# Performance work log

Hardware: AMD Instinct MI355X
Metric: run time of the kernel (lower is better)

Reference implementation:

```python
import jax, jax.numpy as jnp
import numpy as np

B, N, D = 8, 2048, 768
H = 12
HD = D // H
W = 16          # window_size
HOP = 8         # hop_size
GB = N // 2 + 1   # global freq bins = 1025
LB = W // 2 + 1   # local freq bins = 9
NW = (N - W) // HOP + 1  # num windows = 255
EPS_LN = 1e-5


def setup_inputs() -> dict:
    key = jax.random.key(0)
    ks = jax.random.split(key, 12)
    s = 0.02
    return {
        "x": jax.random.normal(ks[0], (B, N, D), dtype=jnp.float32),
        "base_filter_global": jnp.ones((H, GB, 1), jnp.float32),
        "base_filter_local": jnp.ones((H, LB, 1), jnp.float32),
        "modrelu_bias_global": jnp.full((H, GB, 1), -0.1, jnp.float32),
        "modrelu_bias_local": jnp.full((H, LB, 1), -0.1, jnp.float32),
        "w1g": jax.random.normal(ks[1], (D, D), jnp.float32) * s,
        "b1g": jnp.zeros((D,), jnp.float32),
        "w2g": jax.random.normal(ks[2], (D, H * GB), jnp.float32) * s,
        "b2g": jnp.zeros((H * GB,), jnp.float32),
        "w1l": jax.random.normal(ks[3], (D, D), jnp.float32) * s,
        "b1l": jnp.zeros((D,), jnp.float32),
        "w2l": jax.random.normal(ks[4], (D, H * LB), jnp.float32) * s,
        "b2l": jnp.zeros((H * LB,), jnp.float32),
        "fusion_w": jax.random.normal(ks[5], (2,), jnp.float32) * 0.5,
        "ln_gamma": jnp.ones((D,), jnp.float32),
        "ln_beta": jnp.zeros((D,), jnp.float32),
    }


def _modrelu(z, bias):
    # modReLU: ReLU(|z| + b) * z / |z|  (|z| clamped at 1e-6 in denominator)
    a = jnp.abs(z)
    return z * (jax.nn.relu(a + bias) / jnp.maximum(a, 1e-6))


def _hann(w):
    # torch.hann_window default (periodic=True)
    n = jnp.arange(w, dtype=jnp.float32)
    return 0.5 * (1.0 - jnp.cos(2.0 * jnp.pi * n / w))


def reference(x, base_filter_global, base_filter_local, modrelu_bias_global,
              modrelu_bias_local, w1g, b1g, w2g, b2g, w1l, b1l, w2l, b2l,
              fusion_w, ln_gamma, ln_beta):
    b, n, d = x.shape
    x_heads = x.reshape(b, n, H, HD).transpose(0, 2, 1, 3)  # (B,H,N,hd)

    # ---- global branch ----
    Fg = jnp.fft.rfft(x_heads, axis=2, norm='ortho')  # (B,H,GB,hd) complex
    ctx = x.mean(axis=1)  # (B,D)
    mg = jnp.tanh(jax.nn.gelu(ctx @ w1g + b1g, approximate=False) @ w2g + b2g)
    mg = mg.reshape(b, H, GB, 1)
    Fg = Fg * (base_filter_global[None] + mg)
    Fg = _modrelu(Fg, modrelu_bias_global[None])
    x_global = jnp.fft.irfft(Fg, n=n, axis=2, norm='ortho')  # (B,H,N,hd)

    # ---- local (STFT) branch ----
    idx = jnp.arange(NW)[:, None] * HOP + jnp.arange(W)[None, :]  # (NW,W)
    x_win = x_heads[:, :, idx, :]  # (B,H,NW,W,hd)
    w = _hann(W)[None, None, None, :, None]
    x_win = x_win * w
    Fl = jnp.fft.rfft(x_win, axis=3, norm='ortho')  # (B,H,NW,LB,hd)
    ml = jnp.tanh(jax.nn.gelu(ctx @ w1l + b1l, approximate=False) @ w2l + b2l)
    ml = ml.reshape(b, H, 1, LB, 1)
    Fl = Fl * (base_filter_local[None, :, None] + ml)
    Fl = _modrelu(Fl, modrelu_bias_local[None, :, None])
    x_lwin = jnp.fft.irfft(Fl, n=W, axis=3, norm='ortho') * w  # (B,H,NW,W,hd)

    # vectorized overlap-add
    flat_idx = idx.reshape(-1)  # (NW*W,)
    x_local = jnp.zeros((b, H, n, HD), x.dtype).at[:, :, flat_idx, :].add(
        x_lwin.reshape(b, H, NW * W, HD))

    # ---- fuse + residual + layernorm ----
    fused = x_global * fusion_w[0] + x_local * fusion_w[1]  # Linear(2,1,bias=False)
    x_out = fused.transpose(0, 2, 1, 3).reshape(b, n, d)
    y = x + x_out  # dropout is identity at p=0 / eval
    mu = y.mean(axis=-1, keepdims=True)
    var = y.var(axis=-1, keepdims=True)
    return (y - mu) / jnp.sqrt(var + EPS_LN) * ln_gamma + ln_beta
```

## Files before the change

kernel.cpp:

```cpp
#include <hip/hip_runtime.h>
#include <math.h>

#define B_  8
#define N_  2048
#define D_  768
#define H_  12
#define HD_ 64
#define GB_ 1025
#define LB_ 9
#define NW_ 255

#define CBX(i) ((i) + ((i) >> 4))
#define XS(i)  ((i) + ((i) >> 3))

#define C1_ 0.92387953251128674f
#define S1_ 0.38268343236508978f
#define R2_ 0.70710678118654752f

#define FBF(i,k,wr,wi) { const float ar=yr[i],ai=yi[i],br=yr[k],bi=yi[k]; \
  yr[i]=ar+br; yi[i]=ai+bi; const float dr=ar-br, di=ai-bi; \
  yr[k]=fmaf(dr,wr,-(di*(wi))); yi[k]=fmaf(dr,wi,di*(wr)); }
#define FBF1(i,k) { const float ar=yr[i],ai=yi[i],br=yr[k],bi=yi[k]; \
  yr[i]=ar+br; yi[i]=ai+bi; yr[k]=ar-br; yi[k]=ai-bi; }
#define FBFmi(i,k) { const float ar=yr[i],ai=yi[i],br=yr[k],bi=yi[k]; \
  yr[i]=ar+br; yi[i]=ai+bi; yr[k]=ai-bi; yi[k]=br-ar; }

#define IBF(i,k,wr,wi) { const float br=yr[k],bi=yi[k]; \
  const float tr=fmaf(br,wr,-(bi*(wi))), ti=fmaf(br,wi,bi*(wr)); \
  yr[k]=yr[i]-tr; yi[k]=yi[i]-ti; yr[i]+=tr; yi[i]+=ti; }
#define IBF1(i,k) { const float tr=yr[k], ti=yi[k]; \
  yr[k]=yr[i]-tr; yi[k]=yi[i]-ti; yr[i]+=tr; yi[i]+=ti; }
#define IBFpi(i,k) { const float tr=-yi[k], ti=yr[k]; \
  yr[k]=yr[i]-tr; yi[k]=yi[i]-ti; yr[i]+=tr; yi[i]+=ti; }

__device__ __forceinline__ float2 cmulf(float2 a, float2 b) {
  return make_float2(fmaf(a.x, b.x, -(a.y*b.y)), fmaf(a.x, b.y, a.y*b.x));
}
__device__ __forceinline__ float2 caddf(float2 a, float2 b){ return make_float2(a.x+b.x, a.y+b.y); }
__device__ __forceinline__ float2 csubf(float2 a, float2 b){ return make_float2(a.x-b.x, a.y-b.y); }

__global__ __launch_bounds__(256) void k_ctx(const float* __restrict__ x,
                                             float* __restrict__ ctx) {
  const int b = blockIdx.x;
  const int nc = blockIdx.y;
  const int tid = threadIdx.x;
  const int n0 = nc * 64;
  for (int c = tid; c < D_; c += 256) {
    float s = 0.0f;
    #pragma unroll 4
    for (int n = 0; n < 64; ++n)
      s += x[((size_t)(b*N_ + n0 + n))*D_ + c];
    atomicAdd(&ctx[b*D_ + c], s);
  }
}

__global__ __launch_bounds__(256) void k_mlp1(
    const float* __restrict__ ctx,
    const float* __restrict__ w1g, const float* __restrict__ b1g,
    const float* __restrict__ w1l, const float* __restrict__ b1l,
    float* __restrict__ h1g, float* __restrict__ h1l) {
  __shared__ float hs[B_*D_];
  __shared__ float red[4][16][33];
  const int tid = threadIdx.x;
  const bool isl = (blockIdx.y != 0);
  const float* w1 = isl ? w1l : w1g;
  const float* b1 = isl ? b1l : b1g;
  float*       h1 = isl ? h1l : h1g;
  const int j0 = (int)blockIdx.x * 64;

  for (int i = tid; i < B_*D_; i += 256) hs[i] = ctx[i] * (1.0f/(float)N_);
  __syncthreads();

  const int jg    = tid & 15;
  const int slice = tid >> 4;
  const int j     = j0 + jg*4;
  float acc[8][4] = {};
  {
    const float4* w14 = (const float4*)w1;
    const int jc = j >> 2;
    const int i0 = slice*48;
    #pragma unroll 4
    for (int ii = 0; ii < 48; ++ii) {
      const int i = i0 + ii;
      const float4 w = w14[(size_t)i*192 + jc];
      #pragma unroll
      for (int b = 0; b < 8; ++b) {
        const float hv = hs[b*D_ + i];
        acc[b][0] = fmaf(hv, w.x, acc[b][0]);
        acc[b][1] = fmaf(hv, w.y, acc[b][1]);
        acc[b][2] = fmaf(hv, w.z, acc[b][2]);
        acc[b][3] = fmaf(hv, w.w, acc[b][3]);
      }
    }
  }
  #pragma unroll
  for (int b = 0; b < 8; ++b) {
    #pragma unroll
    for (int q = 0; q < 4; ++q) {
      float v = acc[b][q];
      v += __shfl_xor(v, 16, 64);
      v += __shfl_xor(v, 32, 64);
      acc[b][q] = v;
    }
  }
  const int wv = tid >> 6;
  if ((tid & 63) < 16) {
    #pragma unroll
    for (int b = 0; b < 8; ++b)
      #pragma unroll
      for (int q = 0; q < 4; ++q)
        red[wv][jg][b*4+q] = acc[b][q];
  }
  __syncthreads();
  for (int s = tid; s < 512; s += 256) {
    const int jg2 = s >> 5;
    const int v2  = s & 31;
    const int b   = v2 >> 2, q = v2 & 3;
    const int jo  = j0 + jg2*4 + q;
    const float sum = red[0][jg2][v2] + red[1][jg2][v2]
                    + red[2][jg2][v2] + red[3][jg2][v2];
    const float v = sum + b1[jo];
    h1[(size_t)b*D_ + jo] = 0.5f * v * (1.0f + erff(v * 0.70710678118654752f));
  }
}

__global__ __launch_bounds__(256) void k_mlp2(
    const float* __restrict__ h1g, const float* __restrict__ h1l,
    const float* __restrict__ w2g, const float* __restrict__ b2g,
    const float* __restrict__ w2l, const float* __restrict__ b2l,
    float* __restrict__ mg, float* __restrict__ ml) {
  __shared__ float hs[B_*D_];
  __shared__ float red[4][16][33];
  const int tid = threadIdx.x;
  const bool isg = (blockIdx.x < 193);
  const float* h1 = isg ? h1g : h1l;
  const float* w2 = isg ? w2g : w2l;
  const float* b2 = isg ? b2g : b2l;
  float*       mo = isg ? mg  : ml;
  const int Jmax = isg ? (H_*GB_) : (H_*LB_);
  const int j0   = isg ? (int)blockIdx.x*64 : ((int)blockIdx.x-193)*64;

  for (int i = tid; i < B_*D_; i += 256) hs[i] = h1[i];
  __syncthreads();

  const int jg    = tid & 15;
  const int slice = tid >> 4;
  const int j     = j0 + jg*4;
  float acc[8][4] = {};
  if (j < Jmax) {
    const float4* w24 = (const float4*)w2;
    const int jc   = j >> 2;
    const int rowq = Jmax >> 2;
    const int i0   = slice*48;
    #pragma unroll 4
    for (int ii = 0; ii < 48; ++ii) {
      const int i = i0 + ii;
      const float4 w = w24[(size_t)i*rowq + jc];
      #pragma unroll
      for (int b = 0; b < 8; ++b) {
        const float hv = hs[b*D_ + i];
        acc[b][0] = fmaf(hv, w.x, acc[b][0]);
        acc[b][1] = fmaf(hv, w.y, acc[b][1]);
        acc[b][2] = fmaf(hv, w.z, acc[b][2]);
        acc[b][3] = fmaf(hv, w.w, acc[b][3]);
      }
    }
  }
  #pragma unroll
  for (int b = 0; b < 8; ++b) {
    #pragma unroll
    for (int q = 0; q < 4; ++q) {
      float v = acc[b][q];
      v += __shfl_xor(v, 16, 64);
      v += __shfl_xor(v, 32, 64);
      acc[b][q] = v;
    }
  }
  const int wv = tid >> 6;
  if ((tid & 63) < 16) {
    #pragma unroll
    for (int b = 0; b < 8; ++b)
      #pragma unroll
      for (int q = 0; q < 4; ++q)
        red[wv][jg][b*4+q] = acc[b][q];
  }
  __syncthreads();
  for (int s = tid; s < 512; s += 256) {
    const int jg2 = s >> 5;
    const int v2  = s & 31;
    const int b   = v2 >> 2, q = v2 & 3;
    const int jo  = j0 + jg2*4 + q;
    if (jo < Jmax) {
      const float sum = red[0][jg2][v2] + red[1][jg2][v2]
                      + red[2][jg2][v2] + red[3][jg2][v2];
      mo[(size_t)b*Jmax + jo] = tanhf(sum + b2[jo]);
    }
  }
}

__global__ __launch_bounds__(256) void k_spectral(
    const float* __restrict__ x,
    const float* __restrict__ bfg, const float* __restrict__ bfl,
    const float* __restrict__ mbg, const float* __restrict__ mbl,
    const float* __restrict__ mg,  const float* __restrict__ ml,
    const float* __restrict__ fw,  float* __restrict__ fused) {
  __shared__ float2 cb[N_ + (N_>>4)];
  __shared__ float2 tw[1024];
  __shared__ float  xc1[N_ + (N_>>3)], xc2[N_ + (N_>>3)];
  __shared__ float  lf[LB_], lb[LB_];

  const int tid = threadIdx.x;
  const int id  = blockIdx.x;
  const int v_  = (id & 7) * 384 + (id >> 3);
  const int dp  = v_ & 31;
  const int bh  = v_ >> 5;
  const int h   = bh % H_;
  const int b   = bh / H_;
  const int d   = dp * 2;
  const int c   = h*HD_ + d;
  const int col0 = bh*HD_ + d;

  for (int m = tid; m < 1024; m += 256) {
    float s_, c_;
    sincospif(-(float)m * (1.0f/1024.0f), &s_, &c_);
    tw[m] = make_float2(c_, s_);
  }
  if (tid < LB_) {
    lf[tid] = bfl[h*LB_ + tid] + ml[(size_t)b*(H_*LB_) + h*LB_ + tid];
    lb[tid] = mbl[h*LB_ + tid];
  }
  for (int n = tid; n < N_; n += 256) {
    const float2 v = *(const float2*)&x[((size_t)(b*N_ + n))*D_ + c];
    xc1[XS(n)] = v.x; xc2[XS(n)] = v.y;
    cb[CBX(n)] = v;
  }
  __syncthreads();

  #pragma unroll
  for (int sh = 10; sh >= 2; sh -= 2) {
    const int hspan = 1 << sh, hh = hspan >> 1;
    for (int t = tid; t < 512; t += 256) {
      const int p  = t & (hh-1);
      const int g  = t >> (sh-1);
      const int i0 = (g << (sh+1)) | p;
      float2 a = cb[CBX(i0)], bb = cb[CBX(i0+hh)], cc = cb[CBX(i0+hspan)], dd = cb[CBX(i0+hspan+hh)];
      const float2 w1  = tw[p << (10-sh)];
      const float2 w1b = tw[(p+hh) << (10-sh)];
      const float2 w2  = tw[p << (11-sh)];
      float2 ap = caddf(a, cc),  cp = cmulf(csubf(a, cc), w1);
      float2 bp = caddf(bb, dd), dp2 = cmulf(csubf(bb, dd), w1b);
      cb[CBX(i0)]          = caddf(ap, bp);
      cb[CBX(i0+hh)]       = cmulf(csubf(ap, bp), w2);
      cb[CBX(i0+hspan)]    = caddf(cp, dp2);
      cb[CBX(i0+hspan+hh)] = cmulf(csubf(cp, dp2), w2);
    }
    __syncthreads();
  }
  for (int t = tid; t < 1024; t += 256) {
    const int i0 = t << 1;
    float2 a = cb[CBX(i0)], bb = cb[CBX(i0+1)];
    cb[CBX(i0)]   = caddf(a, bb);
    cb[CBX(i0+1)] = csubf(a, bb);
  }
  __syncthreads();

  const float fsc = 0.022097086912079610f;
  {
    const float* mgp = mg + (size_t)b*(H_*GB_) + h*GB_;
    const float* bfp = bfg + h*GB_;
    const float* mbp = mbg + h*GB_;
    for (int k = tid; k < 1024; k += 256) {
      if (k == 0) {
        float2 Z0 = cb[CBX(0)], Zn = cb[CBX(1)];
        float g1 = Z0.x * fsc, g2 = Z0.y * fsc;
        {
          const float filt = bfp[0] + mgp[0], bias = mbp[0];
          g1 *= filt; g2 *= filt;
          float a1 = fabsf(g1); g1 *= fmaxf(a1 + bias, 0.0f) / fmaxf(a1, 1e-6f);
          float a2 = fabsf(g2); g2 *= fmaxf(a2 + bias, 0.0f) / fmaxf(a2, 1e-6f);
        }
        cb[CBX(0)] = make_float2(g1, g2);
        float n1 = Zn.x * fsc, n2 = Zn.y * fsc;
        {
          const float filt = bfp[1024] + mgp[1024], bias = mbp[1024];
          n1 *= filt; n2 *= filt;
          float a1 = fabsf(n1); n1 *= fmaxf(a1 + bias, 0.0f) / fmaxf(a1, 1e-6f);
          float a2 = fabsf(n2); n2 *= fmaxf(a2 + bias, 0.0f) / fmaxf(a2, 1e-6f);
        }
        cb[CBX(1)] = make_float2(n1, n2);
      } else {
        const int ik  = (int)(__brev((unsigned)k) >> 21);
        const int imk = (int)(__brev((unsigned)(2048 - k)) >> 21);
        const float2 Za = cb[CBX(ik)], Zb = cb[CBX(imk)];
        const float hs_ = 0.5f * fsc;
        float f1r = (Za.x + Zb.x) * hs_, f1i = (Za.y - Zb.y) * hs_;
        float f2r = (Za.y + Zb.y) * hs_, f2i = (Zb.x - Za.x) * hs_;
        const float filt = bfp[k] + mgp[k], bias = mbp[k];
        f1r *= filt; f1i *= filt; f2r *= filt; f2i *= filt;
        const float a1 = sqrtf(f1r*f1r + f1i*f1i);
        const float s1 = fmaxf(a1 + bias, 0.0f) / fmaxf(a1, 1e-6f);
        f1r *= s1; f1i *= s1;
        const float a2 = sqrtf(f2r*f2r + f2i*f2i);
        const float s2 = fmaxf(a2 + bias, 0.0f) / fmaxf(a2, 1e-6f);
        f2r *= s2; f2i *= s2;
        cb[CBX(ik)]  = make_float2(f1r - f2i, f1i + f2r);
        cb[CBX(imk)] = make_float2(f1r + f2i, f2r - f1i);
      }
    }
  }
  __syncthreads();

  for (int t = tid; t < 1024; t += 256) {
    const int i0 = t << 1;
    float2 a = cb[CBX(i0)], bb = cb[CBX(i0+1)];
    cb[CBX(i0)]   = caddf(a, bb);
    cb[CBX(i0+1)] = csubf(a, bb);
  }
  __syncthreads();
  #pragma unroll
  for (int sh = 2; sh <= 10; sh += 2) {
    const int hspan = 1 << sh, hh = hspan >> 1;
    for (int t = tid; t < 512; t += 256) {
      const int p  = t & (hh-1);
      const int g  = t >> (sh-1);
      const int i0 = (g << (sh+1)) | p;
      float2 a = cb[CBX(i0)], bb = cb[CBX(i0+hh)], cc = cb[CBX(i0+hspan)], dd = cb[CBX(i0+hspan+hh)];
      float2 w2  = tw[p << (11-sh)];       w2.y  = -w2.y;
      float2 w1  = tw[p << (10-sh)];       w1.y  = -w1.y;
      float2 w1b = tw[(p+hh) << (10-sh)];  w1b.y = -w1b.y;
      float2 t1 = cmulf(bb, w2);
      float2 ap = caddf(a, t1),  bp = csubf(a, t1);
      float2 t2 = cmulf(dd, w2);
      float2 cp = caddf(cc, t2), dp2 = csubf(cc, t2);
      float2 T = cmulf(cp, w1);
      float2 U = cmulf(dp2, w1b);
      cb[CBX(i0)]          = caddf(ap, T);
      cb[CBX(i0+hspan)]    = csubf(ap, T);
      cb[CBX(i0+hh)]       = caddf(bp, U);
      cb[CBX(i0+hspan+hh)] = csubf(bp, U);
    }
    __syncthreads();
  }

  const float HWIN[16] = {0.0f, 0.038060233744356624f, 0.14644660940672624f, 0.30865828381745508f,
                          0.5f, 0.69134171618254492f, 0.85355339059327376f, 0.96193976625564337f,
                          1.0f, 0.96193976625564337f, 0.85355339059327376f, 0.69134171618254492f,
                          0.5f, 0.30865828381745508f, 0.14644660940672624f, 0.038060233744356624f};
  float yr[16], yi[16];
  const int j = tid;
  if (j < NW_) {
    #pragma unroll
    for (int t = 0; t < 16; ++t) {
      yr[t] = xc1[XS(j*8 + t)] * HWIN[t];
      yi[t] = xc2[XS(j*8 + t)] * HWIN[t];
    }
    FBF1(0,8); FBF(1,9,C1_,-S1_); FBF(2,10,R2_,-R2_); FBF(3,11,S1_,-C1_);
    FBFmi(4,12); FBF(5,13,-S1_,-C1_); FBF(6,14,-R2_,-R2_); FBF(7,15,-C1_,-S1_);
    FBF1(0,4); FBF(1,5,R2_,-R2_); FBFmi(2,6); FBF(3,7,-R2_,-R2_);
    FBF1(8,12); FBF(9,13,R2_,-R2_); FBFmi(10,14); FBF(11,15,-R2_,-R2_);
    FBF1(0,2); FBFmi(1,3); FBF1(4,6); FBFmi(5,7);
    FBF1(8,10); FBFmi(9,11); FBF1(12,14); FBFmi(13,15);
    FBF1(0,1); FBF1(2,3); FBF1(4,5); FBF1(6,7);
    FBF1(8,9); FBF1(10,11); FBF1(12,13); FBF1(14,15);
    {
      const int IA[9] = {0,8,4,12,2,10,6,14,1};
      const int IB[9] = {0,15,7,11,3,13,5,9,1};
      #pragma unroll
      for (int l = 0; l <= 8; ++l) {
        const int ia = IA[l], ib = IB[l];
        const float Zar=yr[ia], Zai=yi[ia], Zbr=yr[ib], Zbi=yi[ib];
        float f1r = 0.125f*(Zar+Zbr), f1i = 0.125f*(Zai-Zbi);
        float f2r = 0.125f*(Zai+Zbi), f2i = 0.125f*(Zbr-Zar);
        const float ft = lf[l], bs = lb[l];
        f1r *= ft; f1i *= ft; f2r *= ft; f2i *= ft;
        const float a1 = sqrtf(f1r*f1r + f1i*f1i);
        const float m1 = fmaxf(a1 + bs, 0.0f) / fmaxf(a1, 1e-6f);
        f1r *= m1; f1i *= m1;
        const float a2 = sqrtf(f2r*f2r + f2i*f2i);
        const float m2 = fmaxf(a2 + bs, 0.0f) / fmaxf(a2, 1e-6f);
        f2r *= m2; f2i *= m2;
        yr[ia] = f1r - f2i; yi[ia] = f1i + f2r;
        if (l >= 1 && l <= 7) { yr[ib] = f1r + f2i; yi[ib] = f2r - f1i; }
      }
    }
    IBF1(0,1); IBF1(2,3); IBF1(4,5); IBF1(6,7);
    IBF1(8,9); IBF1(10,11); IBF1(12,13); IBF1(14,15);
    IBF1(0,2); IBFpi(1,3); IBF1(4,6); IBFpi(5,7);
    IBF1(8,10); IBFpi(9,11); IBF1(12,14); IBFpi(13,15);
    IBF1(0,4); IBF(1,5,R2_,R2_); IBFpi(2,6); IBF(3,7,-R2_,R2_);
    IBF1(8,12); IBF(9,13,R2_,R2_); IBFpi(10,14); IBF(11,15,-R2_,R2_);
    IBF1(0,8); IBF(1,9,C1_,S1_); IBF(2,10,R2_,R2_); IBF(3,11,S1_,C1_);
    IBFpi(4,12); IBF(5,13,-S1_,C1_); IBF(6,14,-R2_,R2_); IBF(7,15,-C1_,S1_);
  }
  __syncthreads();
  if (j < NW_ && !(j & 1)) {
    #pragma unroll
    for (int t = 0; t < 16; ++t) {
      const float q = 0.25f * HWIN[t];
      xc1[XS(j*8 + t)] = yr[t] * q;
      xc2[XS(j*8 + t)] = yi[t] * q;
    }
  }
  __syncthreads();
  if (j < NW_ && (j & 1)) {
    #pragma unroll
    for (int t = 0; t < 16; ++t) {
      const float q = 0.25f * HWIN[t];
      xc1[XS(j*8 + t)] += yr[t] * q;
      xc2[XS(j*8 + t)] += yi[t] * q;
    }
  }
  __syncthreads();

  const float fw1 = fw[1];
  const float fwg = fw[0] * fsc;
  float* f0 = fused + (size_t)col0 * N_;
  float* f1 = f0 + N_;
  for (int n = tid; n < N_; n += 256) {
    const float2 v = cb[CBX(n)];
    f0[n] = fwg * v.x + fw1 * xc1[XS(n)];
    f1[n] = fwg * v.y + fw1 * xc2[XS(n)];
  }
}

__global__ __launch_bounds__(256) void k_ln(const float* __restrict__ x,
                                            const float* __restrict__ fused,
                                            const float* __restrict__ gamma,
                                            const float* __restrict__ beta,
                                            float* __restrict__ out) {
  __shared__ float yt[16*776];
  __shared__ float mus[16], rsd[16];
  const int bi = blockIdx.x;
  const int b  = bi >> 7;
  const int n0 = (bi & 127) * 16;
  const int tid = threadIdx.x;

  {
    const float4* x4 = (const float4*)(x + ((size_t)(b*N_ + n0))*D_);
    for (int i = tid; i < 16*D_/4; i += 256) {
      const int nn = i / 192, r = i - nn*192;
      const float4 v = x4[i];
      float* yp = &yt[nn*776 + r*4];
      yp[0] = v.x; yp[1] = v.y; yp[2] = v.z; yp[3] = v.w;
    }
  }
  __syncthreads();
  {
    const float4* fu4 = (const float4*)fused;
    for (int i = tid; i < 16*D_/4; i += 256) {
      const int cc = i >> 2, q = (i & 3) * 4;
      const float4 g = fu4[(((size_t)(b*D_ + cc))*N_ + n0)/4 + (i & 3)];
      yt[(q+0)*776 + cc] += g.x;
      yt[(q+1)*776 + cc] += g.y;
      yt[(q+2)*776 + cc] += g.z;
      yt[(q+3)*776 + cc] += g.w;
    }
  }
  __syncthreads();
  const int nn = tid >> 4, cl = tid & 15;
  float s1 = 0.0f, s2 = 0.0f;
  for (int c = cl; c < D_; c += 16) {
    const float v = yt[nn*776 + c];
    s1 += v; s2 += v*v;
  }
  #pragma unroll
  for (int m = 8; m >= 1; m >>= 1) {
    s1 += __shfl_xor(s1, m, 16);
    s2 += __shfl_xor(s2, m, 16);
  }
  if (cl == 0) {
    const float mu  = s1 * (1.0f/(float)D_);
    const float var = s2 * (1.0f/(float)D_) - mu*mu;
    mus[nn] = mu;
    rsd[nn] = rsqrtf(var + 1e-5f);
  }
  __syncthreads();
  {
    float4* o4 = (float4*)(out + ((size_t)(b*N_ + n0))*D_);
    const float4* g4 = (const float4*)gamma;
    const float4* be4 = (const float4*)beta;
    for (int i = tid; i < 16*D_/4; i += 256) {
      const int nn2 = i / 192, r = i - nn2*192;
      const float mu = mus[nn2], rs = rsd[nn2];
      const float4 gm = g4[r], bt = be4[r];
      const float* yp = &yt[nn2*776 + r*4];
      float4 o;
      o.x = (yp[0] - mu) * rs * gm.x + bt.x;
      o.y = (yp[1] - mu) * rs * gm.y + bt.y;
      o.z = (yp[2] - mu) * rs * gm.z + bt.z;
      o.w = (yp[3] - mu) * rs * gm.w + bt.w;
      o4[i] = o;
    }
  }
}

extern "C" void kernel_launch(void* const* d_in, const int* in_sizes, int n_in,
                              void* d_out, int out_size, void* d_ws, size_t ws_size,
                              hipStream_t stream) {
  const float* x   = (const float*)d_in[0];
  const float* bfg = (const float*)d_in[1];
  const float* bfl = (const float*)d_in[2];
  const float* mbg = (const float*)d_in[3];
  const float* mbl = (const float*)d_in[4];
  const float* w1g = (const float*)d_in[5];
  const float* b1g = (const float*)d_in[6];
  const float* w2g = (const float*)d_in[7];
  const float* b2g = (const float*)d_in[8];
  const float* w1l = (const float*)d_in[9];
  const float* b1l = (const float*)d_in[10];
  const float* w2l = (const float*)d_in[11];
  const float* b2l = (const float*)d_in[12];
  const float* fw  = (const float*)d_in[13];
  const float* gam = (const float*)d_in[14];
  const float* bet = (const float*)d_in[15];
  float* out = (float*)d_out;

  float* ws    = (float*)d_ws;
  float* ctx   = ws;
  float* h1g   = ws + 6144;
  float* h1l   = ws + 12288;
  float* mg    = ws + 18432;
  float* ml    = ws + 116832;
  float* fused = ws + 117696;

  hipMemsetAsync(ctx, 0, (size_t)B_*D_*sizeof(float), stream);
  k_ctx<<<dim3(B_, 32), 256, 0, stream>>>(x, ctx);
  k_mlp1<<<dim3(12, 2), 256, 0, stream>>>(ctx, w1g, b1g, w1l, b1l, h1g, h1l);
  k_mlp2<<<195, 256, 0, stream>>>(h1g, h1l, w2g, b2g, w2l, b2l, mg, ml);
  k_spectral<<<B_*H_*32, 256, 0, stream>>>(x, bfg, bfl, mbg, mbl, mg, ml, fw, fused);
  k_ln<<<B_*N_/16, 256, 0, stream>>>(x, fused, gam, bet, out);
}
```

Baseline: 332.9 us.

## Compute STFT branch in registers before global FFT, overlap-add via shuffles

```diff
diff --git a/kernel.cpp b/kernel.cpp
--- a/kernel.cpp
+++ b/kernel.cpp
@@ -11,7 +11,6 @@
 #define NW_ 255
 
 #define CBX(i) ((i) + ((i) >> 4))
-#define XS(i)  ((i) + ((i) >> 3))
 
 #define C1_ 0.92387953251128674f
 #define S1_ 0.38268343236508978f
@@ -206,7 +205,7 @@
     const float* __restrict__ fw,  float* __restrict__ fused) {
   __shared__ float2 cb[N_ + (N_>>4)];
   __shared__ float2 tw[1024];
-  __shared__ float  xc1[N_ + (N_>>3)], xc2[N_ + (N_>>3)];
+  __shared__ float  t1b[4][8], t2b[4][8];
   __shared__ float  lf[LB_], lb[LB_];
 
   const int tid = threadIdx.x;
@@ -231,10 +230,92 @@
   }
   for (int n = tid; n < N_; n += 256) {
     const float2 v = *(const float2*)&x[((size_t)(b*N_ + n))*D_ + c];
-    xc1[XS(n)] = v.x; xc2[XS(n)] = v.y;
     cb[CBX(n)] = v;
   }
   __syncthreads();
+
+  const float HWIN[16] = {0.0f, 0.038060233744356624f, 0.14644660940672624f, 0.30865828381745508f,
+                          0.5f, 0.69134171618254492f, 0.85355339059327376f, 0.96193976625564337f,
+                          1.0f, 0.96193976625564337f, 0.85355339059327376f, 0.69134171618254492f,
+                          0.5f, 0.30865828381745508f, 0.14644660940672624f, 0.038060233744356624f};
+  float w1a[16], w2a[16];
+  {
+    const int j = tid;
+    if (j < NW_) {
+      float yr[16], yi[16];
+      #pragma unroll
+      for (int t = 0; t < 16; ++t) {
+        const float2 v = cb[CBX(j*8 + t)];
+        yr[t] = v.x * HWIN[t];
+        yi[t] = v.y * HWIN[t];
+      }
+      FBF1(0,8); FBF(1,9,C1_,-S1_); FBF(2,10,R2_,-R2_); FBF(3,11,S1_,-C1_);
+      FBFmi(4,12); FBF(5,13,-S1_,-C1_); FBF(6,14,-R2_,-R2_); FBF(7,15,-C1_,-S1_);
+      FBF1(0,4); FBF(1,5,R2_,-R2_); FBFmi(2,6); FBF(3,7,-R2_,-R2_);
+      FBF1(8,12); FBF(9,13,R2_,-R2_); FBFmi(10,14); FBF(11,15,-R2_,-R2_);
+      FBF1(0,2); FBFmi(1,3); FBF1(4,6); FBFmi(5,7);
+      FBF1(8,10); FBFmi(9,11); FBF1(12,14); FBFmi(13,15);
+      FBF1(0,1); FBF1(2,3); FBF1(4,5); FBF1(6,7);
+      FBF1(8,9); FBF1(10,11); FBF1(12,13); FBF1(14,15);
+      {
+        const int IA[9] = {0,8,4,12,2,10,6,14,1};
+        const int IB[9] = {0,15,7,11,3,13,5,9,1};
+        #pragma unroll
+        for (int l = 0; l <= 8; ++l) {
+          const int ia = IA[l], ib = IB[l];
+          const float Zar=yr[ia], Zai=yi[ia], Zbr=yr[ib], Zbi=yi[ib];
+          float f1r = 0.125f*(Zar+Zbr), f1i = 0.125f*(Zai-Zbi);
+          float f2r = 0.125f*(Zai+Zbi), f2i = 0.125f*(Zbr-Zar);
+          const float ft = lf[l], bs = lb[l];
+          f1r *= ft; f1i *= ft; f2r *= ft; f2i *= ft;
+          const float a1 = sqrtf(f1r*f1r + f1i*f1i);
+          const float m1 = fmaxf(a1 + bs, 0.0f) / fmaxf(a1, 1e-6f);
+          f1r *= m1; f1i *= m1;
+          const float a2 = sqrtf(f2r*f2r + f2i*f2i);
+          const float m2 = fmaxf(a2 + bs, 0.0f) / fmaxf(a2, 1e-6f);
+          f2r *= m2; f2i *= m2;
+          yr[ia] = f1r - f2i; yi[ia] = f1i + f2r;
+          if (l >= 1 && l <= 7) { yr[ib] = f1r + f2i; yi[ib] = f2r - f1i; }
+        }
+      }
+      IBF1(0,1); IBF1(2,3); IBF1(4,5); IBF1(6,7);
+      IBF1(8,9); IBF1(10,11); IBF1(12,13); IBF1(14,15);
+      IBF1(0,2); IBFpi(1,3); IBF1(4,6); IBFpi(5,7);
+      IBF1(8,10); IBFpi(9,11); IBF1(12,14); IBFpi(13,15);
+      IBF1(0,4); IBF(1,5,R2_,R2_); IBFpi(2,6); IBF(3,7,-R2_,R2_);
+      IBF1(8,12); IBF(9,13,R2_,R2_); IBFpi(10,14); IBF(11,15,-R2_,R2_);
+      IBF1(0,8); IBF(1,9,C1_,S1_); IBF(2,10,R2_,R2_); IBF(3,11,S1_,C1_);
+      IBFpi(4,12); IBF(5,13,-S1_,C1_); IBF(6,14,-R2_,R2_); IBF(7,15,-C1_,S1_);
+      #pragma unroll
+      for (int t = 0; t < 16; ++t) {
+        const float q = 0.25f * HWIN[t];
+        w1a[t] = yr[t] * q;
+        w2a[t] = yi[t] * q;
+      }
+    } else {
+      #pragma unroll
+      for (int t = 0; t < 16; ++t) { w1a[t] = 0.0f; w2a[t] = 0.0f; }
+    }
+  }
+  const int lane = tid & 63, wvi = tid >> 6;
+  if (lane == 63 && tid < NW_) {
+    #pragma unroll
+    for (int s = 0; s < 8; ++s) { t1b[wvi][s] = w1a[8+s]; t2b[wvi][s] = w2a[8+s]; }
+  }
+  __syncthreads();
+
+  float r1[8], r2[8];
+  #pragma unroll
+  for (int s = 0; s < 8; ++s) {
+    float p1 = __shfl_up(w1a[s+8], 1, 64);
+    float p2 = __shfl_up(w2a[s+8], 1, 64);
+    if (lane == 0) {
+      p1 = wvi ? t1b[wvi-1][s] : 0.0f;
+      p2 = wvi ? t2b[wvi-1][s] : 0.0f;
+    }
+    r1[s] = w1a[s] + p1;
+    r2[s] = w2a[s] + p2;
+  }
 
   #pragma unroll
   for (int sh = 10; sh >= 2; sh -= 2) {
@@ -342,85 +423,22 @@
     __syncthreads();
   }
 
-  const float HWIN[16] = {0.0f, 0.038060233744356624f, 0.14644660940672624f, 0.30865828381745508f,
-                          0.5f, 0.69134171618254492f, 0.85355339059327376f, 0.96193976625564337f,
-                          1.0f, 0.96193976625564337f, 0.85355339059327376f, 0.69134171618254492f,
-                          0.5f, 0.30865828381745508f, 0.14644660940672624f, 0.038060233744356624f};
-  float yr[16], yi[16];
-  const int j = tid;
-  if (j < NW_) {
-    #pragma unroll
-    for (int t = 0; t < 16; ++t) {
-      yr[t] = xc1[XS(j*8 + t)] * HWIN[t];
-      yi[t] = xc2[XS(j*8 + t)] * HWIN[t];
-    }
-    FBF1(0,8); FBF(1,9,C1_,-S1_); FBF(2,10,R2_,-R2_); FBF(3,11,S1_,-C1_);
-    FBFmi(4,12); FBF(5,13,-S1_,-C1_); FBF(6,14,-R2_,-R2_); FBF(7,15,-C1_,-S1_);
-    FBF1(0,4); FBF(1,5,R2_,-R2_); FBFmi(2,6); FBF(3,7,-R2_,-R2_);
-    FBF1(8,12); FBF(9,13,R2_,-R2_); FBFmi(10,14); FBF(11,15,-R2_,-R2_);
-    FBF1(0,2); FBFmi(1,3); FBF1(4,6); FBFmi(5,7);
-    FBF1(8,10); FBFmi(9,11); FBF1(12,14); FBFmi(13,15);
-    FBF1(0,1); FBF1(2,3); FBF1(4,5); FBF1(6,7);
-    FBF1(8,9); FBF1(10,11); FBF1(12,13); FBF1(14,15);
-    {
-      const int IA[9] = {0,8,4,12,2,10,6,14,1};
-      const int IB[9] = {0,15,7,11,3,13,5,9,1};
-      #pragma unroll
-      for (int l = 0; l <= 8; ++l) {
-        const int ia = IA[l], ib = IB[l];
-        const float Zar=yr[ia], Zai=yi[ia], Zbr=yr[ib], Zbi=yi[ib];
-        float f1r = 0.125f*(Zar+Zbr), f1i = 0.125f*(Zai-Zbi);
-        float f2r = 0.125f*(Zai+Zbi), f2i = 0.125f*(Zbr-Zar);
-        const float ft = lf[l], bs = lb[l];
-        f1r *= ft; f1i *= ft; f2r *= ft; f2i *= ft;
-        const float a1 = sqrtf(f1r*f1r + f1i*f1i);
-        const float m1 = fmaxf(a1 + bs, 0.0f) / fmaxf(a1, 1e-6f);
-        f1r *= m1; f1i *= m1;
-        const float a2 = sqrtf(f2r*f2r + f2i*f2i);
-        const float m2 = fmaxf(a2 + bs, 0.0f) / fmaxf(a2, 1e-6f);
-        f2r *= m2; f2i *= m2;
-        yr[ia] = f1r - f2i; yi[ia] = f1i + f2r;
-        if (l >= 1 && l <= 7) { yr[ib] = f1r + f2i; yi[ib] = f2r - f1i; }
-      }
-    }
-    IBF1(0,1); IBF1(2,3); IBF1(4,5); IBF1(6,7);
-    IBF1(8,9); IBF1(10,11); IBF1(12,13); IBF1(14,15);
-    IBF1(0,2); IBFpi(1,3); IBF1(4,6); IBFpi(5,7);
-    IBF1(8,10); IBFpi(9,11); IBF1(12,14); IBFpi(13,15);
-    IBF1(0,4); IBF(1,5,R2_,R2_); IBFpi(2,6); IBF(3,7,-R2_,R2_);
-    IBF1(8,12); IBF(9,13,R2_,R2_); IBFpi(10,14); IBF(11,15,-R2_,R2_);
-    IBF1(0,8); IBF(1,9,C1_,S1_); IBF(2,10,R2_,R2_); IBF(3,11,S1_,C1_);
-    IBFpi(4,12); IBF(5,13,-S1_,C1_); IBF(6,14,-R2_,R2_); IBF(7,15,-C1_,S1_);
-  }
-  __syncthreads();
-  if (j < NW_ && !(j & 1)) {
-    #pragma unroll
-    for (int t = 0; t < 16; ++t) {
-      const float q = 0.25f * HWIN[t];
-      xc1[XS(j*8 + t)] = yr[t] * q;
-      xc2[XS(j*8 + t)] = yi[t] * q;
-    }
-  }
-  __syncthreads();
-  if (j < NW_ && (j & 1)) {
-    #pragma unroll
-    for (int t = 0; t < 16; ++t) {
-      const float q = 0.25f * HWIN[t];
-      xc1[XS(j*8 + t)] += yr[t] * q;
-      xc2[XS(j*8 + t)] += yi[t] * q;
-    }
-  }
-  __syncthreads();
-
-  const float fw1 = fw[1];
-  const float fwg = fw[0] * fsc;
+  const float fw1v = fw[1];
+  const float fwg  = fw[0] * fsc;
   float* f0 = fused + (size_t)col0 * N_;
-  float* f1 = f0 + N_;
-  for (int n = tid; n < N_; n += 256) {
-    const float2 v = cb[CBX(n)];
-    f0[n] = fwg * v.x + fw1 * xc1[XS(n)];
-    f1[n] = fwg * v.y + fw1 * xc2[XS(n)];
-  }
+  float* f1p = f0 + N_;
+  const int n0 = tid * 8;
+  float v0[8], v1[8];
+  #pragma unroll
+  for (int s = 0; s < 8; ++s) {
+    const float2 g = cb[CBX(n0 + s)];
+    v0[s] = fwg * g.x + fw1v * r1[s];
+    v1[s] = fwg * g.y + fw1v * r2[s];
+  }
+  *(float4*)&f0[n0]    = make_float4(v0[0], v0[1], v0[2], v0[3]);
+  *(float4*)&f0[n0+4]  = make_float4(v0[4], v0[5], v0[6], v0[7]);
+  *(float4*)&f1p[n0]   = make_float4(v1[0], v1[1], v1[2], v1[3]);
+  *(float4*)&f1p[n0+4] = make_float4(v1[4], v1[5], v1[6], v1[7]);
 }
 
 __global__ __launch_bounds__(256) void k_ln(const float* __restrict__ x,
```

New measurement: 312.5 us. -6.1%, faster.
